# Kernel tuning notes

Hardware: AMD Instinct MI355X
Metric: run time of the kernel (lower is better)

Reference implementation:

```python
import jax, jax.numpy as jnp
import numpy as np

NUM_FREQS = 8
TEMPERATURE = 100.0
DOWNSAMPLE = 64
GRID = 8
D_OUT = 512


def fourier_embed(x):
    # x: [M, 2] -> [M, NUM_FREQS*2*2], order: per freq [sin(f*x), cos(f*x)]
    freqs = TEMPERATURE ** (jnp.arange(NUM_FREQS, dtype=jnp.float32) / NUM_FREQS)
    xf = x[:, None, :] * freqs[None, :, None]  # [M, F, 2]
    feats = jnp.stack([jnp.sin(xf), jnp.cos(xf)], axis=2)  # [M, F, 2, 2]
    return feats.reshape(x.shape[0], -1)  # [M, 32]


def mlp(x, W1, b1, W2, b2, W3, b3):
    h = jax.nn.silu(x @ W1 + b1)
    h = jax.nn.silu(h @ W2 + b2)
    return h @ W3 + b3


def scatter_to_grid(drags, emb):
    # drags: [BV, N, 2] (pixel coords), emb: [BV, N, 512]
    BV, N, _ = drags.shape
    r = drags[..., 0].astype(jnp.int32) // DOWNSAMPLE  # [BV, N]
    c = drags[..., 1].astype(jnp.int32) // DOWNSAMPLE
    idx = r * GRID + c  # flat cell index in [0, 64)
    b_idx = jnp.arange(BV)[:, None]
    grid = jnp.zeros((BV, GRID * GRID, D_OUT), emb.dtype).at[b_idx, idx].add(emb)
    # -> [BV, 512, 8, 8]
    return grid.transpose(0, 2, 1).reshape(BV, D_OUT, GRID, GRID)


def setup_inputs() -> dict:
    key = jax.random.key(0)
    ks = jax.random.split(key, 8)
    B, V, N = 8, 8, 1024
    IMG = GRID * DOWNSAMPLE  # 512
    drags_start = jax.random.uniform(ks[0], (B, V, N, 2), jnp.float32) * IMG
    drags_end = jax.random.uniform(ks[1], (B, V, N, 2), jnp.float32) * IMG
    pd = NUM_FREQS * 2 * 2  # 32
    W1 = jax.random.normal(ks[2], (pd, 128), jnp.float32) * (1.0 / np.sqrt(pd))
    b1 = jnp.zeros((128,), jnp.float32)
    W2 = jax.random.normal(ks[3], (128, 256), jnp.float32) * (1.0 / np.sqrt(128))
    b2 = jnp.zeros((256,), jnp.float32)
    W3 = jax.random.normal(ks[4], (256, 512), jnp.float32) * (1.0 / np.sqrt(256))
    b3 = jnp.zeros((512,), jnp.float32)
    return dict(drags_start=drags_start, drags_end=drags_end,
                W1=W1, b1=b1, W2=W2, b2=b2, W3=W3, b3=b3)


def reference(drags_start, drags_end, W1, b1, W2, b2, W3, b3):
    B, V, N, _ = drags_start.shape
    BV = B * V
    ds = drags_start.reshape(BV, N, 2)
    de = drags_end.reshape(BV, N, 2)

    def embed(d):  # [BV, N, 2] -> [BV, N, 512]
        feats = fourier_embed(d.reshape(BV * N, 2))  # no_grad in torch
        return mlp(feats, W1, b1, W2, b2, W3, b3).reshape(BV, N, D_OUT)

    emb_s = embed(ds)
    emb_e = embed(de)
    merge_s = scatter_to_grid(ds, emb_s)
    merge_e = scatter_to_grid(de, emb_e)
    return jnp.concatenate([merge_s, merge_e], axis=1)  # [BV, 1024, 8, 8]
```

## Files before the change

kernel.cpp:

```cpp
#include <hip/hip_runtime.h>
#include <hip/hip_bf16.h>

typedef _Float16 half8 __attribute__((ext_vector_type(8)));
typedef _Float16 half4v __attribute__((ext_vector_type(4)));
typedef float floatx4 __attribute__((ext_vector_type(4)));

__device__ const float FREQS[8] = {
    1.0f, 1.7782794100389228f, 3.1622776601683795f, 5.623413251903491f,
    10.0f, 17.78279410038923f, 31.622776601683793f, 56.23413251903491f};

__device__ inline void fsincos(float m, float& s, float& c) {
  constexpr double I2PI_D = 0.15915494309189533576888376337251;
  constexpr float HI = (float)I2PI_D;
  constexpr float LO = (float)(I2PI_D - (double)HI);
  float k = rintf(m * HI);
  float f = fmaf(m, HI, -k);
  f = fmaf(m, LO, f);
  s = __builtin_amdgcn_sinf(f);
  c = __builtin_amdgcn_cosf(f);
}

__device__ inline float silu(float x) { return x / (1.f + __expf(-x)); }

__global__ __launch_bounds__(256) void prep_weights(
    const float* __restrict__ W1, const float* __restrict__ W2,
    const float* __restrict__ W3, _Float16* __restrict__ W1t,
    _Float16* __restrict__ W2t, _Float16* __restrict__ W3t) {
  int tid = blockIdx.x * blockDim.x + threadIdx.x;
  int stride = gridDim.x * blockDim.x;
  for (int i = tid; i < 128 * 32; i += stride) {
    int n = i >> 5, k = i & 31;
    W1t[i] = (_Float16)W1[k * 128 + n];
  }
  for (int i = tid; i < 256 * 128; i += stride) {
    int n = i >> 7, k = i & 127;
    W2t[i] = (_Float16)W2[k * 256 + n];
  }
  for (int i = tid; i < 512 * 256; i += stride) {
    int n = i >> 8, k = i & 255;
    W3t[i] = (_Float16)W3[k * 512 + n];
  }
}

#define HS 136
__global__ __launch_bounds__(256, 2) void embed_scatter(
    const float* __restrict__ dstart, const float* __restrict__ dend,
    const float* __restrict__ b1, const float* __restrict__ b2,
    const _Float16* __restrict__ W1t, const _Float16* __restrict__ W2t,
    _Float16* __restrict__ partial, int* __restrict__ counts) {
  __shared__ _Float16 h1t[64 * HS];
  __shared__ unsigned char cellb[64];
  __shared__ int hist[64];

  int bid = blockIdx.x;
  int bv = bid >> 3;
  int tsel = (bid >> 2) & 1;
  int pg = bid & 3;
  const float* src = tsel ? dend : dstart;
  int tid = threadIdx.x;
  int lane = tid & 63;
  int w = tid >> 6;
  int ln = lane & 15;
  int q = lane >> 4;

  if (tid < 64) hist[tid] = 0;

  half8 w1f[8];
  floatx4 b1v[8];
  for (int mtW = 0; mtW < 8; mtW++) {
    w1f[mtW] = *(const half8*)&W1t[(mtW * 16 + ln) * 32 + q * 8];
    b1v[mtW] = *(const floatx4*)&b1[mtW * 16 + q * 4];
  }
  half8 w2f[4][4];
  float b2v[4];
  for (int nt = 0; nt < 4; nt++) {
    int n = w * 64 + nt * 16 + ln;
    b2v[nt] = b2[n];
    for (int ks = 0; ks < 4; ks++)
      w2f[nt][ks] = *(const half8*)&W2t[n * 128 + ks * 32 + q * 8];
  }
  floatx4 sacc[4][4];
  for (int mc = 0; mc < 4; mc++)
    for (int nt = 0; nt < 4; nt++) sacc[mc][nt] = (floatx4){0.f, 0.f, 0.f, 0.f};

  float fA = FREQS[2 * q], fB = FREQS[2 * q + 1];
  int pbase = bv * 1024 + pg * 256;
  __syncthreads();

  for (int c = 0; c < 4; c++) {
    int pl = c * 64 + w * 16 + ln;
    float2 xy = *(const float2*)&src[(size_t)(pbase + pl) * 2];
    int cell = ((int)xy.x >> 6) * 8 + ((int)xy.y >> 6);
    if (q == 0) {
      cellb[w * 16 + ln] = (unsigned char)cell;
      atomicAdd(&hist[cell], 1);
    }
    half8 fb;
    {
      float s, cc;
      fsincos(xy.x * fA, s, cc); fb[0] = (_Float16)s; fb[2] = (_Float16)cc;
      fsincos(xy.y * fA, s, cc); fb[1] = (_Float16)s; fb[3] = (_Float16)cc;
      fsincos(xy.x * fB, s, cc); fb[4] = (_Float16)s; fb[6] = (_Float16)cc;
      fsincos(xy.y * fB, s, cc); fb[5] = (_Float16)s; fb[7] = (_Float16)cc;
    }
    for (int mtW = 0; mtW < 8; mtW++) {
      floatx4 cc = __builtin_amdgcn_mfma_f32_16x16x32_f16(w1f[mtW], fb, b1v[mtW], 0, 0, 0);
      half4v hv;
      for (int r = 0; r < 4; r++) hv[r] = (_Float16)silu(cc[r]);
      *(half4v*)&h1t[(w * 16 + ln) * HS + mtW * 16 + q * 4] = hv;
    }
    __syncthreads();
    for (int mt = 0; mt < 4; mt++) {
      half8 af[4];
      for (int ks = 0; ks < 4; ks++)
        af[ks] = *(const half8*)&h1t[(mt * 16 + ln) * HS + ks * 32 + q * 8];
      unsigned cw = *(const unsigned*)&cellb[mt * 16 + q * 4];
      int c0 = cw & 255, c1 = (cw >> 8) & 255, c2i = (cw >> 16) & 255, c3 = cw >> 24;
      half4v ao[4];
      for (int mc = 0; mc < 4; mc++) {
        int m = mc * 16 + ln;
        half4v a;
        a[0] = (c0 == m) ? (_Float16)1.f : (_Float16)0.f;
        a[1] = (c1 == m) ? (_Float16)1.f : (_Float16)0.f;
        a[2] = (c2i == m) ? (_Float16)1.f : (_Float16)0.f;
        a[3] = (c3 == m) ? (_Float16)1.f : (_Float16)0.f;
        ao[mc] = a;
      }
      for (int nt = 0; nt < 4; nt++) {
        floatx4 cc = {b2v[nt], b2v[nt], b2v[nt], b2v[nt]};
        for (int ks = 0; ks < 4; ks++)
          cc = __builtin_amdgcn_mfma_f32_16x16x32_f16(af[ks], w2f[nt][ks], cc, 0, 0, 0);
        half4v hb;
        for (int r = 0; r < 4; r++) hb[r] = (_Float16)silu(cc[r]);
        for (int mc = 0; mc < 4; mc++)
          sacc[mc][nt] = __builtin_amdgcn_mfma_f32_16x16x16f16(ao[mc], hb, sacc[mc][nt], 0, 0, 0);
      }
    }
    __syncthreads();
  }
  for (int mc = 0; mc < 4; mc++)
    for (int nt = 0; nt < 4; nt++)
      for (int r = 0; r < 4; r++) {
        int celly = mc * 16 + q * 4 + r;
        int col = w * 64 + nt * 16 + ln;
        partial[(size_t)bid * 16384 + celly * 256 + col] = (_Float16)sacc[mc][nt][r];
      }
  if (tid < 64) counts[bid * 64 + tid] = hist[tid];
}

#define AS 264
__global__ __launch_bounds__(256) void layer3(
    const _Float16* __restrict__ partial, const int* __restrict__ counts,
    const _Float16* __restrict__ W3t, const float* __restrict__ b3,
    float* __restrict__ out) {
  __shared__ _Float16 a_lds[32 * AS];
  __shared__ float cnt_s[32];
  int mb = blockIdx.x;
  int bvts = mb >> 1;
  int cellbase = (mb & 1) * 32;
  int tid = threadIdx.x;
  {
    int row = tid >> 3;
    int cs = (tid & 7) * 32;
    size_t base = (size_t)(bvts * 4) * 16384 + (size_t)(cellbase + row) * 256 + cs;
    for (int j = 0; j < 32; j += 8) {
      half8 v = *(const half8*)&partial[base + j] +
                *(const half8*)&partial[base + 16384 + j] +
                *(const half8*)&partial[base + 32768 + j] +
                *(const half8*)&partial[base + 49152 + j];
      *(half8*)&a_lds[row * AS + cs + j] = v;
    }
  }
  if (tid < 32) {
    int base = bvts * 4 * 64 + cellbase + tid;
    cnt_s[tid] = (float)(counts[base] + counts[base + 64] + counts[base + 128] + counts[base + 192]);
  }
  __syncthreads();
  int lane = tid & 63, w = tid >> 6, ln = lane & 15, q = lane >> 4;
  half8 af[2][8];
  for (int t = 0; t < 2; t++)
    for (int ks = 0; ks < 8; ks++)
      af[t][ks] = *(const half8*)&a_lds[(t * 16 + ln) * AS + ks * 32 + q * 8];
  float cf[2] = {cnt_s[ln], cnt_s[16 + ln]};
  for (int i = 0; i < 8; i++) {
    int n = w * 128 + i * 16;
    half8 wf[8];
    for (int ks = 0; ks < 8; ks++)
      wf[ks] = *(const half8*)&W3t[(size_t)(n + ln) * 256 + ks * 32 + q * 8];
    floatx4 b3v = *(const floatx4*)&b3[n + q * 4];
    floatx4 acc0 = {0.f, 0.f, 0.f, 0.f}, acc1 = {0.f, 0.f, 0.f, 0.f};
    for (int ks = 0; ks < 8; ks++) {
      acc0 = __builtin_amdgcn_mfma_f32_16x16x32_f16(wf[ks], af[0][ks], acc0, 0, 0, 0);
      acc1 = __builtin_amdgcn_mfma_f32_16x16x32_f16(wf[ks], af[1][ks], acc1, 0, 0, 0);
    }
    for (int r = 0; r < 4; r++) {
      int nn = n + q * 4 + r;
      out[((size_t)(bvts * 512 + nn)) * 64 + cellbase + ln] = acc0[r] + cf[0] * b3v[r];
      out[((size_t)(bvts * 512 + nn)) * 64 + cellbase + 16 + ln] = acc1[r] + cf[1] * b3v[r];
    }
  }
}

extern "C" void kernel_launch(void* const* d_in, const int* in_sizes, int n_in,
                              void* d_out, int out_size, void* d_ws, size_t ws_size,
                              hipStream_t stream) {
  const float* dstart = (const float*)d_in[0];
  const float* dend = (const float*)d_in[1];
  const float* W1 = (const float*)d_in[2];
  const float* b1 = (const float*)d_in[3];
  const float* W2 = (const float*)d_in[4];
  const float* b2 = (const float*)d_in[5];
  const float* W3 = (const float*)d_in[6];
  const float* b3 = (const float*)d_in[7];
  float* out = (float*)d_out;

  char* ws = (char*)d_ws;
  _Float16* W1t = (_Float16*)(ws);
  _Float16* W2t = (_Float16*)(ws + 8192);
  _Float16* W3t = (_Float16*)(ws + 73728);
  _Float16* partial = (_Float16*)(ws + 335872);
  int* counts = (int*)(ws + 335872 + 16777216);

  hipLaunchKernelGGL(prep_weights, dim3(64), dim3(256), 0, stream,
                     W1, W2, W3, W1t, W2t, W3t);
  hipLaunchKernelGGL(embed_scatter, dim3(512), dim3(256), 0, stream,
                     dstart, dend, b1, b2, W1t, W2t, partial, counts);
  hipLaunchKernelGGL(layer3, dim3(256), dim3(256), 0, stream,
                     partial, counts, W3t, b3, out);
}
```

Measured before the change: 137.1 us.

## Widen embed blocks to 512 threads, swizzle partials and W3 into MFMA fragment order

The embed kernel now runs 512 threads per block with 8 waves, each owning 32 layer-2 output columns. W1 and b1 are staged in LDS rather than held in registers, which lowers register pressure to permit higher occupancy. Partial grid sums are written in MFMA-fragment (swizzled) order and W3 is pre-permuted into fragment layout, so layer3 does contiguous per-lane loads. layer3 is split into 512 blocks of 16 cells each. SiLU uses a hardware reciprocal and the one-hot scatter matrix is built with bit packing. The trade-offs are more LDS traffic for W1 fragments and scattered scalar LDS writes in layer3.

```diff
diff --git a/kernel.cpp b/kernel.cpp
--- a/kernel.cpp
+++ b/kernel.cpp
@@ -4,6 +4,7 @@
 typedef _Float16 half8 __attribute__((ext_vector_type(8)));
 typedef _Float16 half4v __attribute__((ext_vector_type(4)));
 typedef float floatx4 __attribute__((ext_vector_type(4)));
+typedef unsigned int uint2v __attribute__((ext_vector_type(2)));
 
 __device__ const float FREQS[8] = {
     1.0f, 1.7782794100389228f, 3.1622776601683795f, 5.623413251903491f,
@@ -20,12 +21,14 @@
   c = __builtin_amdgcn_cosf(f);
 }
 
-__device__ inline float silu(float x) { return x / (1.f + __expf(-x)); }
+__device__ inline float fsilu(float x) {
+  return x * __builtin_amdgcn_rcpf(1.f + __expf(-x));
+}
 
 __global__ __launch_bounds__(256) void prep_weights(
     const float* __restrict__ W1, const float* __restrict__ W2,
     const float* __restrict__ W3, _Float16* __restrict__ W1t,
-    _Float16* __restrict__ W2t, _Float16* __restrict__ W3t) {
+    _Float16* __restrict__ W2t, _Float16* __restrict__ W3f) {
   int tid = blockIdx.x * blockDim.x + threadIdx.x;
   int stride = gridDim.x * blockDim.x;
   for (int i = tid; i < 128 * 32; i += stride) {
@@ -37,101 +40,95 @@
     W2t[i] = (_Float16)W2[k * 256 + n];
   }
   for (int i = tid; i < 512 * 256; i += stride) {
-    int n = i >> 8, k = i & 255;
-    W3t[i] = (_Float16)W3[k * 512 + n];
+    int k = i >> 9, n = i & 511;
+    int it = n >> 4, ln = n & 15, ks = k >> 5, q = (k >> 3) & 3, j = k & 7;
+    W3f[((size_t)(it * 8 + ks) * 64 + q * 16 + ln) * 8 + j] = (_Float16)W3[i];
   }
 }
 
 #define HS 136
-__global__ __launch_bounds__(256, 2) void embed_scatter(
+__global__ __launch_bounds__(512, 4) void embed_scatter(
     const float* __restrict__ dstart, const float* __restrict__ dend,
     const float* __restrict__ b1, const float* __restrict__ b2,
     const _Float16* __restrict__ W1t, const _Float16* __restrict__ W2t,
-    _Float16* __restrict__ partial, int* __restrict__ counts) {
-  __shared__ _Float16 h1t[64 * HS];
-  __shared__ unsigned char cellb[64];
+    _Float16* __restrict__ swz, int* __restrict__ counts) {
+  __shared__ _Float16 h1t[128 * HS];
+  __shared__ _Float16 W1lds[4096];
+  __shared__ float b1lds[128];
+  __shared__ unsigned char cellb[128];
   __shared__ int hist[64];
 
   int bid = blockIdx.x;
-  int bv = bid >> 3;
-  int tsel = (bid >> 2) & 1;
-  int pg = bid & 3;
+  int bv = bid >> 3, tsel = (bid >> 2) & 1, pg = bid & 3;
   const float* src = tsel ? dend : dstart;
   int tid = threadIdx.x;
-  int lane = tid & 63;
-  int w = tid >> 6;
-  int ln = lane & 15;
-  int q = lane >> 4;
-
+  int lane = tid & 63, w = tid >> 6, ln = lane & 15, q = lane >> 4;
+
+  *(half8*)&W1lds[tid * 8] = *(const half8*)&W1t[tid * 8];
+  if (tid < 128) b1lds[tid] = b1[tid];
   if (tid < 64) hist[tid] = 0;
 
-  half8 w1f[8];
-  floatx4 b1v[8];
-  for (int mtW = 0; mtW < 8; mtW++) {
-    w1f[mtW] = *(const half8*)&W1t[(mtW * 16 + ln) * 32 + q * 8];
-    b1v[mtW] = *(const floatx4*)&b1[mtW * 16 + q * 4];
-  }
-  half8 w2f[4][4];
-  float b2v[4];
-  for (int nt = 0; nt < 4; nt++) {
-    int n = w * 64 + nt * 16 + ln;
+  half8 w2f[2][4];
+  float b2v[2];
+  for (int nt = 0; nt < 2; nt++) {
+    int n = w * 32 + nt * 16 + ln;
     b2v[nt] = b2[n];
     for (int ks = 0; ks < 4; ks++)
       w2f[nt][ks] = *(const half8*)&W2t[n * 128 + ks * 32 + q * 8];
   }
-  floatx4 sacc[4][4];
+  floatx4 sacc[4][2];
   for (int mc = 0; mc < 4; mc++)
-    for (int nt = 0; nt < 4; nt++) sacc[mc][nt] = (floatx4){0.f, 0.f, 0.f, 0.f};
+    for (int nt = 0; nt < 2; nt++) sacc[mc][nt] = (floatx4){0.f, 0.f, 0.f, 0.f};
 
   float fA = FREQS[2 * q], fB = FREQS[2 * q + 1];
   int pbase = bv * 1024 + pg * 256;
   __syncthreads();
 
-  for (int c = 0; c < 4; c++) {
-    int pl = c * 64 + w * 16 + ln;
+  for (int c = 0; c < 2; c++) {
+    int pl = c * 128 + w * 16 + ln;
     float2 xy = *(const float2*)&src[(size_t)(pbase + pl) * 2];
-    int cell = ((int)xy.x >> 6) * 8 + ((int)xy.y >> 6);
     if (q == 0) {
+      int cell = ((int)xy.x >> 6) * 8 + ((int)xy.y >> 6);
       cellb[w * 16 + ln] = (unsigned char)cell;
       atomicAdd(&hist[cell], 1);
     }
     half8 fb;
     {
-      float s, cc;
-      fsincos(xy.x * fA, s, cc); fb[0] = (_Float16)s; fb[2] = (_Float16)cc;
-      fsincos(xy.y * fA, s, cc); fb[1] = (_Float16)s; fb[3] = (_Float16)cc;
-      fsincos(xy.x * fB, s, cc); fb[4] = (_Float16)s; fb[6] = (_Float16)cc;
-      fsincos(xy.y * fB, s, cc); fb[5] = (_Float16)s; fb[7] = (_Float16)cc;
+      float s, cc2;
+      fsincos(xy.x * fA, s, cc2); fb[0] = (_Float16)s; fb[2] = (_Float16)cc2;
+      fsincos(xy.y * fA, s, cc2); fb[1] = (_Float16)s; fb[3] = (_Float16)cc2;
+      fsincos(xy.x * fB, s, cc2); fb[4] = (_Float16)s; fb[6] = (_Float16)cc2;
+      fsincos(xy.y * fB, s, cc2); fb[5] = (_Float16)s; fb[7] = (_Float16)cc2;
     }
     for (int mtW = 0; mtW < 8; mtW++) {
-      floatx4 cc = __builtin_amdgcn_mfma_f32_16x16x32_f16(w1f[mtW], fb, b1v[mtW], 0, 0, 0);
+      half8 w1f = *(const half8*)&W1lds[(mtW * 16 + ln) * 32 + q * 8];
+      floatx4 c1 = *(const floatx4*)&b1lds[mtW * 16 + q * 4];
+      c1 = __builtin_amdgcn_mfma_f32_16x16x32_f16(w1f, fb, c1, 0, 0, 0);
       half4v hv;
-      for (int r = 0; r < 4; r++) hv[r] = (_Float16)silu(cc[r]);
+      for (int r = 0; r < 4; r++) hv[r] = (_Float16)fsilu(c1[r]);
       *(half4v*)&h1t[(w * 16 + ln) * HS + mtW * 16 + q * 4] = hv;
     }
     __syncthreads();
-    for (int mt = 0; mt < 4; mt++) {
+    for (int mt = 0; mt < 8; mt++) {
       half8 af[4];
       for (int ks = 0; ks < 4; ks++)
         af[ks] = *(const half8*)&h1t[(mt * 16 + ln) * HS + ks * 32 + q * 8];
       unsigned cw = *(const unsigned*)&cellb[mt * 16 + q * 4];
-      int c0 = cw & 255, c1 = (cw >> 8) & 255, c2i = (cw >> 16) & 255, c3 = cw >> 24;
+      unsigned c0 = cw & 255, c1i = (cw >> 8) & 255, c2i = (cw >> 16) & 255, c3i = cw >> 24;
       half4v ao[4];
       for (int mc = 0; mc < 4; mc++) {
-        int m = mc * 16 + ln;
-        half4v a;
-        a[0] = (c0 == m) ? (_Float16)1.f : (_Float16)0.f;
-        a[1] = (c1 == m) ? (_Float16)1.f : (_Float16)0.f;
-        a[2] = (c2i == m) ? (_Float16)1.f : (_Float16)0.f;
-        a[3] = (c3 == m) ? (_Float16)1.f : (_Float16)0.f;
-        ao[mc] = a;
+        unsigned m = mc * 16 + ln;
+        unsigned d0 = (c0 == m ? 0x3C00u : 0u) | (c1i == m ? 0x3C000000u : 0u);
+        unsigned d1 = (c2i == m ? 0x3C00u : 0u) | (c3i == m ? 0x3C000000u : 0u);
+        uint2v u = {d0, d1};
+        ao[mc] = __builtin_bit_cast(half4v, u);
       }
-      for (int nt = 0; nt < 4; nt++) {
+      for (int nt = 0; nt < 2; nt++) {
         floatx4 cc = {b2v[nt], b2v[nt], b2v[nt], b2v[nt]};
         for (int ks = 0; ks < 4; ks++)
           cc = __builtin_amdgcn_mfma_f32_16x16x32_f16(af[ks], w2f[nt][ks], cc, 0, 0, 0);
         half4v hb;
-        for (int r = 0; r < 4; r++) hb[r] = (_Float16)silu(cc[r]);
+        for (int r = 0; r < 4; r++) hb[r] = (_Float16)fsilu(cc[r]);
         for (int mc = 0; mc < 4; mc++)
           sacc[mc][nt] = __builtin_amdgcn_mfma_f32_16x16x16f16(ao[mc], hb, sacc[mc][nt], 0, 0, 0);
       }
@@ -139,65 +136,58 @@
     __syncthreads();
   }
   for (int mc = 0; mc < 4; mc++)
-    for (int nt = 0; nt < 4; nt++)
-      for (int r = 0; r < 4; r++) {
-        int celly = mc * 16 + q * 4 + r;
-        int col = w * 64 + nt * 16 + ln;
-        partial[(size_t)bid * 16384 + celly * 256 + col] = (_Float16)sacc[mc][nt][r];
-      }
+    for (int nt = 0; nt < 2; nt++) {
+      half4v hv;
+      for (int r = 0; r < 4; r++) hv[r] = (_Float16)sacc[mc][nt][r];
+      *(half4v*)&swz[((((size_t)bid * 4 + mc) * 16 + w * 2 + nt) * 64 + lane) * 4] = hv;
+    }
   if (tid < 64) counts[bid * 64 + tid] = hist[tid];
 }
 
 #define AS 264
 __global__ __launch_bounds__(256) void layer3(
-    const _Float16* __restrict__ partial, const int* __restrict__ counts,
-    const _Float16* __restrict__ W3t, const float* __restrict__ b3,
+    const _Float16* __restrict__ swz, const int* __restrict__ counts,
+    const _Float16* __restrict__ W3f, const float* __restrict__ b3,
     float* __restrict__ out) {
-  __shared__ _Float16 a_lds[32 * AS];
-  __shared__ float cnt_s[32];
-  int mb = blockIdx.x;
-  int bvts = mb >> 1;
-  int cellbase = (mb & 1) * 32;
+  __shared__ _Float16 a_lds[16 * AS];
+  __shared__ float cnt_s[16];
+  int bb = blockIdx.x;
+  int bvts = bb >> 2, cq = bb & 3;
   int tid = threadIdx.x;
-  {
-    int row = tid >> 3;
-    int cs = (tid & 7) * 32;
-    size_t base = (size_t)(bvts * 4) * 16384 + (size_t)(cellbase + row) * 256 + cs;
-    for (int j = 0; j < 32; j += 8) {
-      half8 v = *(const half8*)&partial[base + j] +
-                *(const half8*)&partial[base + 16384 + j] +
-                *(const half8*)&partial[base + 32768 + j] +
-                *(const half8*)&partial[base + 49152 + j];
-      *(half8*)&a_lds[row * AS + cs + j] = v;
-    }
-  }
-  if (tid < 32) {
-    int base = bvts * 4 * 64 + cellbase + tid;
-    cnt_s[tid] = (float)(counts[base] + counts[base + 64] + counts[base + 128] + counts[base + 192]);
+  for (int it = 0; it < 4; it++) {
+    int cc = it * 256 + tid;
+    int wn = cc >> 6, lane2 = cc & 63, q2 = lane2 >> 4, ln2 = lane2 & 15;
+    size_t base = ((size_t)bvts * 16 + cq) * 1024 + cc;
+    half4v s = (*(const half4v*)&swz[base * 4] +
+                *(const half4v*)&swz[(base + 4096) * 4]) +
+               (*(const half4v*)&swz[(base + 8192) * 4] +
+                *(const half4v*)&swz[(base + 12288) * 4]);
+    int col = wn * 16 + ln2;
+    for (int r = 0; r < 4; r++) a_lds[(q2 * 4 + r) * AS + col] = s[r];
+  }
+  if (tid < 16) {
+    int base = bvts * 4 * 64 + cq * 16 + tid;
+    cnt_s[tid] = (float)(counts[base] + counts[base + 64] +
+                         counts[base + 128] + counts[base + 192]);
   }
   __syncthreads();
   int lane = tid & 63, w = tid >> 6, ln = lane & 15, q = lane >> 4;
-  half8 af[2][8];
-  for (int t = 0; t < 2; t++)
-    for (int ks = 0; ks < 8; ks++)
-      af[t][ks] = *(const half8*)&a_lds[(t * 16 + ln) * AS + ks * 32 + q * 8];
-  float cf[2] = {cnt_s[ln], cnt_s[16 + ln]};
-  for (int i = 0; i < 8; i++) {
-    int n = w * 128 + i * 16;
+  half8 af[8];
+  for (int ks = 0; ks < 8; ks++)
+    af[ks] = *(const half8*)&a_lds[ln * AS + ks * 32 + q * 8];
+  float cntf = cnt_s[ln];
+  for (int ii = 0; ii < 8; ii++) {
+    int i = w * 8 + ii;
     half8 wf[8];
     for (int ks = 0; ks < 8; ks++)
-      wf[ks] = *(const half8*)&W3t[(size_t)(n + ln) * 256 + ks * 32 + q * 8];
-    floatx4 b3v = *(const floatx4*)&b3[n + q * 4];
-    floatx4 acc0 = {0.f, 0.f, 0.f, 0.f}, acc1 = {0.f, 0.f, 0.f, 0.f};
-    for (int ks = 0; ks < 8; ks++) {
-      acc0 = __builtin_amdgcn_mfma_f32_16x16x32_f16(wf[ks], af[0][ks], acc0, 0, 0, 0);
-      acc1 = __builtin_amdgcn_mfma_f32_16x16x32_f16(wf[ks], af[1][ks], acc1, 0, 0, 0);
-    }
-    for (int r = 0; r < 4; r++) {
-      int nn = n + q * 4 + r;
-      out[((size_t)(bvts * 512 + nn)) * 64 + cellbase + ln] = acc0[r] + cf[0] * b3v[r];
-      out[((size_t)(bvts * 512 + nn)) * 64 + cellbase + 16 + ln] = acc1[r] + cf[1] * b3v[r];
-    }
+      wf[ks] = *(const half8*)&W3f[((size_t)(i * 8 + ks) * 64 + lane) * 8];
+    floatx4 b3v = *(const floatx4*)&b3[i * 16 + q * 4];
+    floatx4 acc = {0.f, 0.f, 0.f, 0.f};
+    for (int ks = 0; ks < 8; ks++)
+      acc = __builtin_amdgcn_mfma_f32_16x16x32_f16(wf[ks], af[ks], acc, 0, 0, 0);
+    for (int r = 0; r < 4; r++)
+      out[((size_t)bvts * 512 + i * 16 + q * 4 + r) * 64 + cq * 16 + ln] =
+          acc[r] + cntf * b3v[r];
   }
 }
 
@@ -217,14 +207,14 @@
   char* ws = (char*)d_ws;
   _Float16* W1t = (_Float16*)(ws);
   _Float16* W2t = (_Float16*)(ws + 8192);
-  _Float16* W3t = (_Float16*)(ws + 73728);
-  _Float16* partial = (_Float16*)(ws + 335872);
+  _Float16* W3f = (_Float16*)(ws + 73728);
+  _Float16* swz = (_Float16*)(ws + 335872);
   int* counts = (int*)(ws + 335872 + 16777216);
 
   hipLaunchKernelGGL(prep_weights, dim3(64), dim3(256), 0, stream,
-                     W1, W2, W3, W1t, W2t, W3t);
-  hipLaunchKernelGGL(embed_scatter, dim3(512), dim3(256), 0, stream,
-                     dstart, dend, b1, b2, W1t, W2t, partial, counts);
-  hipLaunchKernelGGL(layer3, dim3(256), dim3(256), 0, stream,
-                     partial, counts, W3t, b3, out);
-}
+                     W1, W2, W3, W1t, W2t, W3f);
+  hipLaunchKernelGGL(embed_scatter, dim3(512), dim3(512), 0, stream,
+                     dstart, dend, b1, b2, W1t, W2t, swz, counts);
+  hipLaunchKernelGGL(layer3, dim3(512), dim3(256), 0, stream,
+                     swz, counts, W3f, b3, out);
+}
```

New measurement: 119.1 us. 13.1% less time.
